# Kernel optimization log

Measured on AMD Instinct MI355X. Metric: run time of the kernel, lower is better.

Reference implementation:

```python
import jax, jax.numpy as jnp
import numpy as np

N_NODES = 50000
N_EDGES = 600000
N_GRAPHS = 500
IN_DIM = 64
LATENT = [128, 128, 128]
N_CLASSES = 10
N_PROTO_PER_CLASS = 5
N_PROTO = N_CLASSES * N_PROTO_PER_CLASS
GRAPH_SIZE = 10
PROTO_DIM = LATENT[-1]  # single 'mean' readout
EPS = 1e-4


def setup_inputs() -> dict:
    key = jax.random.key(0)
    ks = jax.random.split(key, 12)
    x = jax.random.normal(ks[0], (N_NODES, IN_DIM), dtype=jnp.float32)
    edge_index = jax.random.randint(ks[1], (2, N_EDGES), 0, N_NODES, dtype=jnp.int64)
    batch = jnp.sort(jax.random.randint(ks[2], (N_NODES,), 0, N_GRAPHS, dtype=jnp.int64))
    # GCN layer params (glorot-ish scaling)
    def lin(k, din, dout):
        s = (6.0 / (din + dout)) ** 0.5
        return jax.random.uniform(k, (din, dout), jnp.float32, -s, s)
    W0 = lin(ks[3], IN_DIM, LATENT[0]); b0 = jnp.zeros((LATENT[0],), jnp.float32)
    W1 = lin(ks[4], LATENT[0], LATENT[1]); b1 = jnp.zeros((LATENT[1],), jnp.float32)
    W2 = lin(ks[5], LATENT[1], LATENT[2]); b2 = jnp.zeros((LATENT[2],), jnp.float32)
    s = (6.0 / (GRAPH_SIZE + PROTO_DIM)) ** 0.5
    proto_node_emb = jax.random.uniform(ks[6], (N_PROTO, GRAPH_SIZE, PROTO_DIM), jnp.float32, -s, s)
    # last layer: +1 on correct-class connections, -0.5 on incorrect (set_last_layer_incorrect_connection)
    proto_class = jnp.arange(N_PROTO) // N_PROTO_PER_CLASS  # [P]
    ident = (proto_class[None, :] == jnp.arange(N_CLASSES)[:, None]).astype(jnp.float32)  # [C,P]
    last_w = ident * 1.0 + (1.0 - ident) * (-0.5)
    return {"x": x, "edge_index": edge_index, "batch": batch,
            "W0": W0, "b0": b0, "W1": W1, "b1": b1, "W2": W2, "b2": b2,
            "proto_node_emb": proto_node_emb, "last_w": last_w}


def _gcn_forward(x, edge_index, batch, W0, b0, W1, b1, W2, b2, proto_node_emb, last_w):
    src, dst = edge_index[0], edge_index[1]
    # symmetric normalization with self-loops: deg_i = 1 + in_degree(i)
    deg = 1.0 + jax.ops.segment_sum(jnp.ones((N_EDGES,), jnp.float32), dst, num_segments=N_NODES)
    dis = jax.lax.rsqrt(deg)  # [N]
    norm = dis[src] * dis[dst]  # [E]

    def gcn_layer(h, W, b):
        hw = h @ W  # [N,d]
        agg = jax.ops.segment_sum(hw[src] * norm[:, None], dst, num_segments=N_NODES)
        agg = agg + hw * (dis * dis)[:, None]  # self-loop contribution (norm = 1/deg)
        return agg + b

    h = jax.nn.relu(gcn_layer(x, W0, b0))
    h = jax.nn.relu(gcn_layer(h, W1, b1))
    h = jax.nn.relu(gcn_layer(h, W2, b2))  # node_emb [N, 128]

    # mean readout per graph
    counts = jax.ops.segment_sum(jnp.ones((N_NODES,), jnp.float32), batch, num_segments=N_GRAPHS)
    gsum = jax.ops.segment_sum(h, batch, num_segments=N_GRAPHS)
    graph_emb = gsum / jnp.maximum(counts, 1.0)[:, None]  # [B, 128]

    # prototype graph embeddings via mean readout over prototype nodes
    proto_graph = proto_node_emb.mean(axis=1)  # [P, 128]

    # squared L2 distances [B, P]
    d2 = (jnp.sum(graph_emb ** 2, axis=1)[:, None]
          + jnp.sum(proto_graph ** 2, axis=1)[None, :]
          - 2.0 * graph_emb @ proto_graph.T)
    d2 = jnp.maximum(d2, 0.0)
    sim = jnp.log((d2 + 1.0) / (d2 + EPS))  # [B, P]

    logits = sim @ last_w.T  # [B, C]
    return logits


def reference(x, edge_index, batch, W0, b0, W1, b1, W2, b2, proto_node_emb, last_w):
    return _gcn_forward(x, edge_index, batch, W0, b0, W1, b1, W2, b2, proto_node_emb, last_w)
```

## Files before the change

### kernel.cpp

```cpp
#include <hip/hip_runtime.h>
#include <hip/hip_fp16.h>

#define N_NODES   50000
#define N_EDGES   600000
#define N_GRAPHS  500
#define IN_DIM    64
#define D         128
#define N_CLASSES 10
#define N_PROTO   50
#define GRAPH_SZ  10
#define EPS_F     1e-4f
#define NC4       (N_NODES * IN_DIM / 4)
#define GRP8      ((N_NODES + 7) / 8)
#define G16_TILES (N_NODES / 16)
#define BKT       64

typedef _Float16 half4_t __attribute__((ext_vector_type(4)));
typedef _Float16 half8_t __attribute__((ext_vector_type(8)));
typedef float    f32x4   __attribute__((ext_vector_type(4)));

struct Params {
    const float* x; const int* esrc; const int* edst; const int* bat;
    const float* W0; const float* b0; const float* W1; const float* b1;
    const float* W2; const float* b2; const float* pe; const float* lw;
    float* out;
    _Float16 *bufA, *bufB, *xs, *Bp0, *Bp1, *Bp2;
    float *pg;
    int *src_sorted, *indeg;
};

__device__ __forceinline__ float dis_of(const int* __restrict__ indeg, int n) {
    return rsqrtf(1.0f + (float)indeg[n]);
}

__device__ __forceinline__ void pack_one(const float* __restrict__ W,
                                         _Float16* __restrict__ Bp, int nks, int t) {
    int j = t & 7, l = (t >> 3) & 63;
    int rest = t >> 9;
    int s = rest % nks, c = rest / nks;
    int k = s * 32 + (l >> 4) * 8 + j;
    int col = c * 16 + (l & 15);
    Bp[t] = (_Float16)W[k * D + col];
}

__global__ void kw_p0(Params P) {
    int i = blockIdx.x * 256 + threadIdx.x;
    if (i < N_NODES) { P.indeg[i] = 0; return; }
    i -= N_NODES;
    if (i < 8192)  { pack_one(P.W0, P.Bp0, IN_DIM / 32, i); return; }
    i -= 8192;
    if (i < 16384) { pack_one(P.W1, P.Bp1, D / 32, i); return; }
    i -= 16384;
    if (i < 16384) { pack_one(P.W2, P.Bp2, D / 32, i); return; }
    i -= 16384;
    if (i < N_PROTO * D) {
        int p = i >> 7, j = i & 127;
        float s = 0.f;
#pragma unroll
        for (int g = 0; g < GRAPH_SZ; ++g) s += P.pe[((size_t)p * GRAPH_SZ + g) * D + j];
        P.pg[i] = s * (1.0f / GRAPH_SZ);
    }
}

__global__ void kw_cfc(Params P) {
    int t = blockIdx.x * 256 + threadIdx.x;
    if (t < N_EDGES) {
        int d = P.edst[t];
        int r = atomicAdd(&P.indeg[d], 1);
        if (r < BKT) P.src_sorted[(d << 6) + r] = P.esrc[t];
    }
    if (t < NC4) {
        float4 v = ((const float4*)P.x)[t];
        half4_t h = { (_Float16)v.x, (_Float16)v.y, (_Float16)v.z, (_Float16)v.w };
        ((half4_t*)P.xs)[t] = h;
    }
}

__global__ __launch_bounds__(256, 8) void kw_a0g01(Params P) {
    __shared__ _Float16 xa_t[16][72];
    __shared__ _Float16 h1_t[16][136];
    int tid = threadIdx.x;
    int row0 = blockIdx.x * 16;
    int grp = tid >> 5, lane16 = tid & 15, hf = (tid >> 4) & 1;
    int j4 = lane16 * 4;

#pragma unroll
    for (int iter = 0; iter < 2; ++iter) {
        int nrel = iter * 8 + grp;
        int node = row0 + nrel;
        int cnt = P.indeg[node];
        int base = node << 6;
        float a0 = 0.f, a1 = 0.f, a2 = 0.f, a3 = 0.f;
        int k = hf;
        if (k < cnt) {
            int sc = P.src_sorted[base + k];
            float dc = dis_of(P.indeg, sc);
            half4_t vc = *(const half4_t*)&P.xs[(size_t)sc * IN_DIM + j4];
            for (k += 2; k < cnt; k += 2) {
                int sn = P.src_sorted[base + k];
                float dn = dis_of(P.indeg, sn);
                half4_t vn = *(const half4_t*)&P.xs[(size_t)sn * IN_DIM + j4];
                a0 = fmaf((float)vc[0], dc, a0);
                a1 = fmaf((float)vc[1], dc, a1);
                a2 = fmaf((float)vc[2], dc, a2);
                a3 = fmaf((float)vc[3], dc, a3);
                vc = vn; dc = dn;
            }
            a0 = fmaf((float)vc[0], dc, a0);
            a1 = fmaf((float)vc[1], dc, a1);
            a2 = fmaf((float)vc[2], dc, a2);
            a3 = fmaf((float)vc[3], dc, a3);
        }
        a0 += __shfl_xor(a0, 16);
        a1 += __shfl_xor(a1, 16);
        a2 += __shfl_xor(a2, 16);
        a3 += __shfl_xor(a3, 16);
        if (hf == 0) {
            half4_t hv = *(const half4_t*)&P.xs[(size_t)node * IN_DIM + j4];
            float dd = rsqrtf(1.0f + (float)cnt);
            half4_t r = { (_Float16)((fmaf((float)hv[0], dd, a0)) * dd),
                          (_Float16)((fmaf((float)hv[1], dd, a1)) * dd),
                          (_Float16)((fmaf((float)hv[2], dd, a2)) * dd),
                          (_Float16)((fmaf((float)hv[3], dd, a3)) * dd) };
            *(half4_t*)&xa_t[nrel][j4] = r;
        }
    }
    __syncthreads();

    int wave = tid >> 6, lane = tid & 63;
    int l15 = lane & 15;
    int kof = (lane >> 4) * 8;
    int rb  = (lane >> 4) * 4;
    {
        half8_t af0 = *(const half8_t*)&xa_t[l15][kof];
        half8_t af1 = *(const half8_t*)&xa_t[l15][32 + kof];
        f32x4 acc[2];
        acc[0] = (f32x4){0.f, 0.f, 0.f, 0.f};
        acc[1] = (f32x4){0.f, 0.f, 0.f, 0.f};
#pragma unroll
        for (int cc = 0; cc < 2; ++cc) {
            int c = wave * 2 + cc;
            half8_t b0f = *(const half8_t*)&P.Bp0[(size_t)((c * 2 + 0) * 64 + lane) * 8];
            half8_t b1f = *(const half8_t*)&P.Bp0[(size_t)((c * 2 + 1) * 64 + lane) * 8];
            acc[cc] = __builtin_amdgcn_mfma_f32_16x16x32_f16(af0, b0f, acc[cc], 0, 0, 0);
            acc[cc] = __builtin_amdgcn_mfma_f32_16x16x32_f16(af1, b1f, acc[cc], 0, 0, 0);
        }
#pragma unroll
        for (int cc = 0; cc < 2; ++cc) {
            int col = (wave * 2 + cc) * 16 + l15;
            float bv = P.b0[col];
#pragma unroll
            for (int r = 0; r < 4; ++r)
                h1_t[rb + r][col] = (_Float16)fmaxf(acc[cc][r] + bv, 0.f);
        }
    }
    __syncthreads();

    {
        half8_t af[4];
#pragma unroll
        for (int s = 0; s < 4; ++s)
            af[s] = *(const half8_t*)&h1_t[l15][s * 32 + kof];
        f32x4 acc[2];
        acc[0] = (f32x4){0.f, 0.f, 0.f, 0.f};
        acc[1] = (f32x4){0.f, 0.f, 0.f, 0.f};
#pragma unroll
        for (int cc = 0; cc < 2; ++cc) {
            int c = wave * 2 + cc;
#pragma unroll
            for (int s = 0; s < 4; ++s) {
                half8_t bf = *(const half8_t*)&P.Bp1[(size_t)((c * 4 + s) * 64 + lane) * 8];
                acc[cc] = __builtin_amdgcn_mfma_f32_16x16x32_f16(af[s], bf, acc[cc], 0, 0, 0);
            }
        }
        float dsc[4];
#pragma unroll
        for (int r = 0; r < 4; ++r) dsc[r] = dis_of(P.indeg, row0 + rb + r);
#pragma unroll
        for (int cc = 0; cc < 2; ++cc) {
            int col = (wave * 2 + cc) * 16 + l15;
#pragma unroll
            for (int r = 0; r < 4; ++r)
                P.bufA[(size_t)(row0 + rb + r) * D + col] = (_Float16)(acc[cc][r] * dsc[r]);
        }
    }
}

__global__ __launch_bounds__(256, 8) void kw_g1g2(Params P) {
    __shared__ _Float16 h2_t[16][136];
    int tid = threadIdx.x;
    int row0 = blockIdx.x * 16;
    int grp = tid >> 5, lane16 = tid & 15, hf = (tid >> 4) & 1;
    int j8 = lane16 * 8;

#pragma unroll
    for (int iter = 0; iter < 2; ++iter) {
        int nrel = iter * 8 + grp;
        int node = row0 + nrel;
        int cnt = P.indeg[node];
        int base = node << 6;
        float a[8] = {0.f, 0.f, 0.f, 0.f, 0.f, 0.f, 0.f, 0.f};
        int k = hf;
        if (k < cnt) {
            int sc = P.src_sorted[base + k];
            half8_t vc = *(const half8_t*)&P.bufA[(size_t)sc * D + j8];
            for (k += 2; k < cnt; k += 2) {
                int sn = P.src_sorted[base + k];
                half8_t vn = *(const half8_t*)&P.bufA[(size_t)sn * D + j8];
#pragma unroll
                for (int j = 0; j < 8; ++j) a[j] += (float)vc[j];
                vc = vn;
            }
#pragma unroll
            for (int j = 0; j < 8; ++j) a[j] += (float)vc[j];
        }
#pragma unroll
        for (int j = 0; j < 8; ++j) a[j] += __shfl_xor(a[j], 16);
        if (hf == 0) {
            float dd = rsqrtf(1.0f + (float)cnt);
            half8_t hv = *(const half8_t*)&P.bufA[(size_t)node * D + j8];
            half8_t r;
#pragma unroll
            for (int j = 0; j < 8; ++j)
                r[j] = (_Float16)fmaxf((a[j] + (float)hv[j]) * dd + P.b1[j8 + j], 0.f);
            *(half8_t*)&h2_t[nrel][j8] = r;
        }
    }
    __syncthreads();

    int wave = tid >> 6, lane = tid & 63;
    int l15 = lane & 15;
    int kof = (lane >> 4) * 8;
    int rb  = (lane >> 4) * 4;
    half8_t af[4];
#pragma unroll
    for (int s = 0; s < 4; ++s)
        af[s] = *(const half8_t*)&h2_t[l15][s * 32 + kof];
    f32x4 acc[2];
    acc[0] = (f32x4){0.f, 0.f, 0.f, 0.f};
    acc[1] = (f32x4){0.f, 0.f, 0.f, 0.f};
#pragma unroll
    for (int cc = 0; cc < 2; ++cc) {
        int c = wave * 2 + cc;
#pragma unroll
        for (int s = 0; s < 4; ++s) {
            half8_t bf = *(const half8_t*)&P.Bp2[(size_t)((c * 4 + s) * 64 + lane) * 8];
            acc[cc] = __builtin_amdgcn_mfma_f32_16x16x32_f16(af[s], bf, acc[cc], 0, 0, 0);
        }
    }
    float dsc[4];
#pragma unroll
    for (int r = 0; r < 4; ++r) dsc[r] = dis_of(P.indeg, row0 + rb + r);
#pragma unroll
    for (int cc = 0; cc < 2; ++cc) {
        int col = (wave * 2 + cc) * 16 + l15;
#pragma unroll
        for (int r = 0; r < 4; ++r)
            P.bufB[(size_t)(row0 + rb + r) * D + col] = (_Float16)(acc[cc][r] * dsc[r]);
    }
}

__global__ __launch_bounds__(256, 8) void kw_gather2(Params P) {
    int node = blockIdx.x * 8 + (threadIdx.x >> 5);
    if (node >= N_NODES) return;
    int lane16 = threadIdx.x & 15;
    int hf = (threadIdx.x >> 4) & 1;
    int j8 = lane16 * 8;
    int cnt = P.indeg[node];
    int base = node << 6;
    float a[8] = {0.f, 0.f, 0.f, 0.f, 0.f, 0.f, 0.f, 0.f};
    int k = hf;
    if (k < cnt) {
        int sc = P.src_sorted[base + k];
        half8_t vc = *(const half8_t*)&P.bufB[(size_t)sc * D + j8];
        for (k += 2; k < cnt; k += 2) {
            int sn = P.src_sorted[base + k];
            half8_t vn = *(const half8_t*)&P.bufB[(size_t)sn * D + j8];
#pragma unroll
            for (int j = 0; j < 8; ++j) a[j] += (float)vc[j];
            vc = vn;
        }
#pragma unroll
        for (int j = 0; j < 8; ++j) a[j] += (float)vc[j];
    }
#pragma unroll
    for (int j = 0; j < 8; ++j) a[j] += __shfl_xor(a[j], 16);
    if (hf == 0) {
        float dd = rsqrtf(1.0f + (float)cnt);
        half8_t hv = *(const half8_t*)&P.bufB[(size_t)node * D + j8];
        half8_t r;
#pragma unroll
        for (int j = 0; j < 8; ++j)
            r[j] = (_Float16)fmaxf((a[j] + (float)hv[j]) * dd + P.b2[j8 + j], 0.f);
        *(half8_t*)&P.bufA[(size_t)node * D + j8] = r;
    }
}

__global__ void kw_readout(Params P) {
    __shared__ int sh[2];
    __shared__ float red[4][D];
    __shared__ float gs[D];
    __shared__ float sim[N_PROTO];
    const _Float16* h = P.bufA;
    int g = blockIdx.x;
    if (threadIdx.x == 0) {
        int lo = 0, hi = N_NODES;
        while (lo < hi) { int m = (lo + hi) >> 1; if (P.bat[m] < g) lo = m + 1; else hi = m; }
        sh[0] = lo;
        hi = N_NODES;
        while (lo < hi) { int m = (lo + hi) >> 1; if (P.bat[m] < g + 1) lo = m + 1; else hi = m; }
        sh[1] = lo;
    }
    __syncthreads();
    int s0 = sh[0], s1 = sh[1];
    int col = threadIdx.x & 127;
    int part = threadIdx.x >> 7;
    float sum = 0.f;
    for (int n = s0 + part; n < s1; n += 4) sum += (float)h[(size_t)n * D + col];
    red[part][col] = sum;
    __syncthreads();
    if (part == 0)
        gs[col] = (sum + red[1][col] + red[2][col] + red[3][col])
                  / fmaxf((float)(s1 - s0), 1.0f);
    __syncthreads();
    int t = threadIdx.x;
    if (t < N_PROTO * 8) {
        int p = t >> 3, sub = t & 7;
        const float* q = P.pg + (size_t)p * D;
        float d2 = 0.f;
        int j0 = sub * 16;
#pragma unroll
        for (int j = 0; j < 16; ++j) {
            float df = gs[j0 + j] - q[j0 + j];
            d2 = fmaf(df, df, d2);
        }
        d2 += __shfl_xor(d2, 1);
        d2 += __shfl_xor(d2, 2);
        d2 += __shfl_xor(d2, 4);
        if (sub == 0) sim[p] = logf((d2 + 1.0f) / (d2 + EPS_F));
    }
    __syncthreads();
    if (t < N_CLASSES) {
        float s = 0.f;
#pragma unroll
        for (int p = 0; p < N_PROTO; ++p) s = fmaf(sim[p], P.lw[t * N_PROTO + p], s);
        P.out[(size_t)g * N_CLASSES + t] = s;
    }
}

extern "C" void kernel_launch(void* const* d_in, const int* in_sizes, int n_in,
                              void* d_out, int out_size, void* d_ws, size_t ws_size,
                              hipStream_t stream) {
    Params P;
    P.x    = (const float*)d_in[0];
    P.esrc = (const int*)d_in[1];
    P.edst = (const int*)d_in[1] + N_EDGES;
    P.bat  = (const int*)d_in[2];
    P.W0 = (const float*)d_in[3];  P.b0 = (const float*)d_in[4];
    P.W1 = (const float*)d_in[5];  P.b1 = (const float*)d_in[6];
    P.W2 = (const float*)d_in[7];  P.b2 = (const float*)d_in[8];
    P.pe = (const float*)d_in[9];  P.lw = (const float*)d_in[10];
    P.out = (float*)d_out;

    char* wsb = (char*)d_ws;
    P.bufA = (_Float16*)wsb;  wsb += (size_t)N_NODES * D * 2;
    P.bufB = (_Float16*)wsb;  wsb += (size_t)N_NODES * D * 2;
    P.xs   = (_Float16*)wsb;  wsb += (size_t)N_NODES * IN_DIM * 2;
    P.Bp0  = (_Float16*)wsb;  wsb += (size_t)IN_DIM * D * 2;
    P.Bp1  = (_Float16*)wsb;  wsb += (size_t)D * D * 2;
    P.Bp2  = (_Float16*)wsb;  wsb += (size_t)D * D * 2;
    P.pg   = (float*)wsb;     wsb += (size_t)N_PROTO * D * 4;
    P.src_sorted = (int*)wsb; wsb += (size_t)N_NODES * BKT * 4;
    P.indeg      = (int*)wsb; wsb += (size_t)N_NODES * 4;

    const int TB = 256;
    int p0_blocks = (N_NODES + 8192 + 16384 + 16384 + N_PROTO * D + TB - 1) / TB;
    int cfc_blocks = (NC4 + TB - 1) / TB;

    kw_p0<<<p0_blocks, TB, 0, stream>>>(P);
    kw_cfc<<<cfc_blocks, TB, 0, stream>>>(P);
    kw_a0g01<<<G16_TILES, TB, 0, stream>>>(P);
    kw_g1g2<<<G16_TILES, TB, 0, stream>>>(P);
    kw_gather2<<<GRP8, TB, 0, stream>>>(P);
    kw_readout<<<N_GRAPHS, 512, 0, stream>>>(P);
}
```

Measured before the change: 146.2 us.

## Replace global-atomic edge bucketing with two-pass coarse histogram and LDS sort

Edge bucketing by destination no longer does one global atomicAdd per edge on a 50k-entry degree array. It now runs in two passes. First, a block-local LDS histogram per 256-node coarse bucket with one global atomic per bucket per block. Second, a per-bucket kernel that ranks edges in shared memory and writes src_sorted and indeg. The x-to-fp16 conversion moves into the prep kernel. This trades scattered global atomics for an extra launch and an intermediate coarse buffer, and it relies on node ids fitting in 16 bits and on at most 4096 edges per coarse bucket.

```diff
diff --git a/kernel.cpp b/kernel.cpp
--- a/kernel.cpp
+++ b/kernel.cpp
@@ -14,6 +14,11 @@
 #define GRP8      ((N_NODES + 7) / 8)
 #define G16_TILES (N_NODES / 16)
 #define BKT       64
+#define NCB       196
+#define CBCAP     4096
+#define HBLK      392
+#define EPB       ((N_EDGES + HBLK - 1) / HBLK)
+#define KPT       ((EPB + 255) / 256)
 
 typedef _Float16 half4_t __attribute__((ext_vector_type(4)));
 typedef _Float16 half8_t __attribute__((ext_vector_type(8)));
@@ -26,7 +31,7 @@
     float* out;
     _Float16 *bufA, *bufB, *xs, *Bp0, *Bp1, *Bp2;
     float *pg;
-    int *src_sorted, *indeg;
+    int *src_sorted, *indeg, *coarse, *cursor;
 };
 
 __device__ __forceinline__ float dis_of(const int* __restrict__ indeg, int n) {
@@ -45,8 +50,8 @@
 
 __global__ void kw_p0(Params P) {
     int i = blockIdx.x * 256 + threadIdx.x;
-    if (i < N_NODES) { P.indeg[i] = 0; return; }
-    i -= N_NODES;
+    if (i < NCB) { P.cursor[i] = 0; return; }
+    i -= NCB;
     if (i < 8192)  { pack_one(P.W0, P.Bp0, IN_DIM / 32, i); return; }
     i -= 8192;
     if (i < 16384) { pack_one(P.W1, P.Bp1, D / 32, i); return; }
@@ -59,21 +64,67 @@
 #pragma unroll
         for (int g = 0; g < GRAPH_SZ; ++g) s += P.pe[((size_t)p * GRAPH_SZ + g) * D + j];
         P.pg[i] = s * (1.0f / GRAPH_SZ);
-    }
-}
-
-__global__ void kw_cfc(Params P) {
-    int t = blockIdx.x * 256 + threadIdx.x;
-    if (t < N_EDGES) {
-        int d = P.edst[t];
-        int r = atomicAdd(&P.indeg[d], 1);
-        if (r < BKT) P.src_sorted[(d << 6) + r] = P.esrc[t];
-    }
-    if (t < NC4) {
-        float4 v = ((const float4*)P.x)[t];
+        return;
+    }
+    i -= N_PROTO * D;
+    if (i < NC4) {
+        float4 v = ((const float4*)P.x)[i];
         half4_t h = { (_Float16)v.x, (_Float16)v.y, (_Float16)v.z, (_Float16)v.w };
-        ((half4_t*)P.xs)[t] = h;
-    }
+        ((half4_t*)P.xs)[i] = h;
+    }
+}
+
+__global__ __launch_bounds__(256) void kw_hist(Params P) {
+    __shared__ int hcnt[NCB];
+    __shared__ int hbase[NCB];
+    int tid = threadIdx.x;
+    for (int i = tid; i < NCB; i += 256) hcnt[i] = 0;
+    __syncthreads();
+    int e0 = blockIdx.x * EPB;
+    int e1 = e0 + EPB; if (e1 > N_EDGES) e1 = N_EDGES;
+    int lr[KPT], pb[KPT], pl[KPT];
+#pragma unroll
+    for (int i = 0; i < KPT; ++i) {
+        int e = e0 + i * 256 + tid;
+        lr[i] = -1;
+        if (e < e1) {
+            int d = P.edst[e];
+            int b = d >> 8;
+            pb[i] = b;
+            pl[i] = P.esrc[e] | ((d & 255) << 16);
+            lr[i] = atomicAdd(&hcnt[b], 1);
+        }
+    }
+    __syncthreads();
+    for (int i = tid; i < NCB; i += 256)
+        hbase[i] = hcnt[i] ? atomicAdd(&P.cursor[i], hcnt[i]) : 0;
+    __syncthreads();
+#pragma unroll
+    for (int i = 0; i < KPT; ++i) {
+        if (lr[i] >= 0) {
+            int pos = hbase[pb[i]] + lr[i];
+            if (pos < CBCAP) P.coarse[(pb[i] << 12) + pos] = pl[i];
+        }
+    }
+}
+
+__global__ __launch_bounds__(256) void kw_sort(Params P) {
+    __shared__ int edges[CBCAP];
+    __shared__ int nrank[256];
+    int b = blockIdx.x, tid = threadIdx.x;
+    int total = P.cursor[b]; if (total > CBCAP) total = CBCAP;
+    for (int i = tid; i < total; i += 256) edges[i] = P.coarse[(b << 12) + i];
+    nrank[tid] = 0;
+    __syncthreads();
+    for (int i = tid; i < total; i += 256) {
+        int pl = edges[i];
+        int dl = pl >> 16;
+        int r = atomicAdd(&nrank[dl], 1);
+        if (r < BKT) P.src_sorted[(((b << 8) | dl) << 6) + r] = pl & 0xFFFF;
+    }
+    __syncthreads();
+    int node = (b << 8) + tid;
+    if (node < N_NODES) P.indeg[node] = nrank[tid];
 }
 
 __global__ __launch_bounds__(256, 8) void kw_a0g01(Params P) {
@@ -371,14 +422,17 @@
     P.Bp2  = (_Float16*)wsb;  wsb += (size_t)D * D * 2;
     P.pg   = (float*)wsb;     wsb += (size_t)N_PROTO * D * 4;
     P.src_sorted = (int*)wsb; wsb += (size_t)N_NODES * BKT * 4;
+    P.coarse     = (int*)wsb; wsb += (size_t)NCB * CBCAP * 4;
     P.indeg      = (int*)wsb; wsb += (size_t)N_NODES * 4;
+    P.cursor     = (int*)wsb; wsb += (size_t)NCB * 4;
 
     const int TB = 256;
-    int p0_blocks = (N_NODES + 8192 + 16384 + 16384 + N_PROTO * D + TB - 1) / TB;
-    int cfc_blocks = (NC4 + TB - 1) / TB;
+    int p0_threads = NCB + 8192 + 16384 + 16384 + N_PROTO * D + NC4;
+    int p0_blocks  = (p0_threads + TB - 1) / TB;
 
     kw_p0<<<p0_blocks, TB, 0, stream>>>(P);
-    kw_cfc<<<cfc_blocks, TB, 0, stream>>>(P);
+    kw_hist<<<HBLK, TB, 0, stream>>>(P);
+    kw_sort<<<NCB, TB, 0, stream>>>(P);
     kw_a0g01<<<G16_TILES, TB, 0, stream>>>(P);
     kw_g1g2<<<G16_TILES, TB, 0, stream>>>(P);
     kw_gather2<<<GRP8, TB, 0, stream>>>(P);
```

Measured after the change: 134.6 us. -8.0%, faster.
